# Kernel tuning notes

Measured on AMD Instinct MI355X. Metric: run time of the kernel, lower is better.

## Reference

```python
import jax, jax.numpy as jnp
import numpy as np

N_USER, N_ITEM, N_REL = 200000, 100000, 64
DIM = 64
S_UU = S_UI = S_IU = S_II = 8
BATCH = 65536
MAX_RATING = 5.0


def setup_inputs() -> dict:
    key = jax.random.key(0)
    ks = jax.random.split(key, 24)
    inp = {}
    # query batch
    inp['u'] = jax.random.randint(ks[0], (BATCH,), 0, N_USER)
    inp['v'] = jax.random.randint(ks[1], (BATCH,), 0, N_ITEM)
    # embedding tables (init std=0.8 as in the torch code)
    inp['usr_feat'] = 0.8 * jax.random.normal(ks[2], (N_USER, DIM), jnp.float32)
    inp['item_feat'] = 0.8 * jax.random.normal(ks[3], (N_ITEM, DIM), jnp.float32)
    inp['rel_feat'] = 0.8 * jax.random.normal(ks[4], (N_REL, DIM), jnp.float32)
    # precomputed sampled neighbor tables (built once in __init__ in the original)
    inp['neigh_uu'] = jax.random.randint(ks[5], (N_USER, S_UU), 0, N_USER)
    inp['neigh_uu_st'] = jax.random.uniform(ks[6], (N_USER, S_UU), jnp.float32)
    inp['neigh_ui'] = jax.random.randint(ks[7], (N_USER, S_UI), 0, N_ITEM)
    inp['neigh_ui_rat'] = MAX_RATING * jax.random.uniform(ks[8], (N_USER, S_UI), jnp.float32)
    inp['neigh_ui_vot'] = jax.random.uniform(ks[9], (N_USER, S_UI), jnp.float32)
    inp['neigh_ui_tim'] = jax.random.uniform(ks[10], (N_USER, S_UI), jnp.float32)
    inp['neigh_iu'] = jax.random.randint(ks[11], (N_ITEM, S_IU), 0, N_USER)
    inp['neigh_iu_rat'] = MAX_RATING * jax.random.uniform(ks[12], (N_ITEM, S_IU), jnp.float32)
    inp['neigh_iu_vot'] = jax.random.uniform(ks[13], (N_ITEM, S_IU), jnp.float32)
    inp['neigh_iu_tim'] = jax.random.uniform(ks[14], (N_ITEM, S_IU), jnp.float32)
    inp['neigh_ii'] = jax.random.randint(ks[15], (N_ITEM, S_II), 0, N_ITEM)
    inp['neigh_ir'] = jax.random.randint(ks[16], (N_ITEM, S_II), 0, N_REL)
    # aggregator transforms (one per side)
    sc = 1.0 / np.sqrt(DIM)
    inp['Wu'] = sc * jax.random.normal(ks[17], (DIM, DIM), jnp.float32)
    inp['bu'] = jnp.zeros((DIM,), jnp.float32)
    inp['Wv'] = sc * jax.random.normal(ks[18], (DIM, DIM), jnp.float32)
    inp['bv'] = jnp.zeros((DIM,), jnp.float32)
    return inp


def reference(u, v, usr_feat, item_feat, rel_feat,
              neigh_uu, neigh_uu_st, neigh_ui, neigh_ui_rat, neigh_ui_vot, neigh_ui_tim,
              neigh_iu, neigh_iu_rat, neigh_iu_vot, neigh_iu_tim, neigh_ii, neigh_ir,
              Wu, bu, Wv, bv):
    u_emb = usr_feat[u]                                   # [B, D]
    v_emb = item_feat[v]                                  # [B, D]

    # ---- user-side aggregation ----
    # social neighbors, weighted by softmax over social tie strength
    uu_nei = usr_feat[neigh_uu[u]]                        # [B, S, D]
    w_uu = jax.nn.softmax(neigh_uu_st[u], axis=-1)        # [B, S]
    agg_uu = jnp.einsum('bs,bsd->bd', w_uu, uu_nei)
    # interacted items, weighted by rating * vote * time recency
    ui_nei = item_feat[neigh_ui[u]]                       # [B, S, D]
    s_ui = neigh_ui_rat[u] * neigh_ui_vot[u] * neigh_ui_tim[u]
    w_ui = jax.nn.softmax(s_ui, axis=-1)
    agg_ui = jnp.einsum('bs,bsd->bd', w_ui, ui_nei)
    user_h = jax.nn.relu((u_emb + agg_uu + agg_ui) @ Wu + bu)

    # ---- item-side aggregation ----
    # users who interacted with the item, weighted like above
    iu_nei = usr_feat[neigh_iu[v]]                        # [B, S, D]
    s_iu = neigh_iu_rat[v] * neigh_iu_vot[v] * neigh_iu_tim[v]
    w_iu = jax.nn.softmax(s_iu, axis=-1)
    agg_iu = jnp.einsum('bs,bsd->bd', w_iu, iu_nei)
    # KG neighbors with user-relation attention (KGCN-style)
    ii_nei = item_feat[neigh_ii[v]]                       # [B, S, D]
    rel = rel_feat[neigh_ir[v]]                           # [B, S, D]
    att = jnp.einsum('bd,bsd->bs', u_emb, rel)            # user-relation score
    w_ii = jax.nn.softmax(att, axis=-1)
    agg_ii = jnp.einsum('bs,bsd->bd', w_ii, ii_nei)
    item_h = jax.nn.relu((v_emb + agg_iu + agg_ii) @ Wv + bv)

    # rating prediction
    score = jax.nn.sigmoid(jnp.sum(user_h * item_h, axis=-1)) * MAX_RATING
    return score
```

## Files before the change

kernel.cpp:

```cpp
#include <hip/hip_runtime.h>
#include <math.h>

constexpr int DIM = 64;
constexpr int S = 8;
constexpr int WPB = 4;
constexpr int BLOCK = WPB * 64;
constexpr int GRID = 2048;

constexpr int N_USER = 200000;
constexpr int N_ITEM = 100000;
constexpr size_t USR16_BYTES  = (size_t)N_USER * DIM * 2;
constexpr size_t ITEM16_BYTES = (size_t)N_ITEM * DIM * 2;
constexpr size_t WS_NEEDED    = USR16_BYTES + ITEM16_BYTES;

typedef __attribute__((ext_vector_type(8))) __bf16 bf16x8;
typedef __attribute__((ext_vector_type(4))) float  f32x4;
typedef __attribute__((ext_vector_type(8))) float     f32x8;
typedef __attribute__((ext_vector_type(8))) _Float16  f16x8;

#define LDS_FENCE() asm volatile("s_waitcnt lgkmcnt(0)" ::: "memory")
#define SCHED_PIN() __builtin_amdgcn_sched_barrier(0)

template <int CTRL>
__device__ __forceinline__ float dppx(float x) {
    return __builtin_bit_cast(float,
        __builtin_amdgcn_mov_dpp(__builtin_bit_cast(int, x), CTRL, 0xf, 0xf, true));
}
#define XOR1 0xB1
#define XOR2 0x4E

__device__ __forceinline__ unsigned pk_bf16(float a, float b) {
    unsigned ua = __builtin_bit_cast(unsigned, a);
    unsigned ub = __builtin_bit_cast(unsigned, b);
    ua = (ua + 0x8000u) >> 16;
    ub = (ub + 0x8000u) & 0xffff0000u;
    return ua | ub;
}

__device__ __forceinline__ void octet_softmax(float sc, float* wout) {
    float m = sc;
    m = fmaxf(m, dppx<XOR1>(m));
    m = fmaxf(m, dppx<XOR2>(m));
    m = fmaxf(m, __shfl_xor(m, 4));
    float e = __expf(sc - m);
    float s = e;
    s += dppx<XOR1>(s);
    s += dppx<XOR2>(s);
    s += __shfl_xor(s, 4);
    float w = e / s;
    #pragma unroll
    for (int k = 0; k < 8; k++) wout[k] = __shfl(w, k);
}

__device__ __forceinline__ void matvec_h(
    float xv, int lane, unsigned short* xw,
    const bf16x8* xa00, const bf16x8* xa01,
    const bf16x8* xa10, const bf16x8* xa11,
    const unsigned* bf,
    float b0, float b1, float b2, float b3,
    float& h0, float& h1, float& h2, float& h3)
{
    LDS_FENCE();
    const unsigned xb = __builtin_bit_cast(unsigned, xv);
    const unsigned hb = (xb + 0x8000u) & 0xffff0000u;
    const float xl = xv - __builtin_bit_cast(float, hb);
    xw[lane]      = (unsigned short)(hb >> 16);
    xw[64 + lane] = (unsigned short)((__builtin_bit_cast(unsigned, xl) + 0x8000u) >> 16);
    LDS_FENCE();

    f32x4 a0 = {0.f, 0.f, 0.f, 0.f};
    f32x4 a1 = a0, a2 = a0, a3 = a0;

    {
        const bf16x8 ah = *xa00, al = *xa01;
        const bf16x8 w0 = *(const bf16x8*)(bf);
        const bf16x8 w1 = *(const bf16x8*)(bf + 256);
        const bf16x8 w2 = *(const bf16x8*)(bf + 512);
        const bf16x8 w3 = *(const bf16x8*)(bf + 768);
        a0 = __builtin_amdgcn_mfma_f32_16x16x32_bf16(ah, w0, a0, 0, 0, 0);
        a0 = __builtin_amdgcn_mfma_f32_16x16x32_bf16(al, w0, a0, 0, 0, 0);
        a1 = __builtin_amdgcn_mfma_f32_16x16x32_bf16(ah, w1, a1, 0, 0, 0);
        a1 = __builtin_amdgcn_mfma_f32_16x16x32_bf16(al, w1, a1, 0, 0, 0);
        a2 = __builtin_amdgcn_mfma_f32_16x16x32_bf16(ah, w2, a2, 0, 0, 0);
        a2 = __builtin_amdgcn_mfma_f32_16x16x32_bf16(al, w2, a2, 0, 0, 0);
        a3 = __builtin_amdgcn_mfma_f32_16x16x32_bf16(ah, w3, a3, 0, 0, 0);
        a3 = __builtin_amdgcn_mfma_f32_16x16x32_bf16(al, w3, a3, 0, 0, 0);
    }
    {
        const bf16x8 ah = *xa10, al = *xa11;
        const bf16x8 w0 = *(const bf16x8*)(bf + 1024);
        const bf16x8 w1 = *(const bf16x8*)(bf + 1280);
        const bf16x8 w2 = *(const bf16x8*)(bf + 1536);
        const bf16x8 w3 = *(const bf16x8*)(bf + 1792);
        a0 = __builtin_amdgcn_mfma_f32_16x16x32_bf16(ah, w0, a0, 0, 0, 0);
        a0 = __builtin_amdgcn_mfma_f32_16x16x32_bf16(al, w0, a0, 0, 0, 0);
        a1 = __builtin_amdgcn_mfma_f32_16x16x32_bf16(ah, w1, a1, 0, 0, 0);
        a1 = __builtin_amdgcn_mfma_f32_16x16x32_bf16(al, w1, a1, 0, 0, 0);
        a2 = __builtin_amdgcn_mfma_f32_16x16x32_bf16(ah, w2, a2, 0, 0, 0);
        a2 = __builtin_amdgcn_mfma_f32_16x16x32_bf16(al, w2, a2, 0, 0, 0);
        a3 = __builtin_amdgcn_mfma_f32_16x16x32_bf16(ah, w3, a3, 0, 0, 0);
        a3 = __builtin_amdgcn_mfma_f32_16x16x32_bf16(al, w3, a3, 0, 0, 0);
    }

    h0 = fmaxf(a0[0] + b0, 0.f);
    h1 = fmaxf(a1[0] + b1, 0.f);
    h2 = fmaxf(a2[0] + b2, 0.f);
    h3 = fmaxf(a3[0] + b3, 0.f);
}

__global__ __launch_bounds__(256)
void cvt16_kernel(const float* __restrict__ usr_feat, const float* __restrict__ item_feat,
                  _Float16* __restrict__ usr16, _Float16* __restrict__ item16,
                  int n8u, int n8t)
{
    const int i = blockIdx.x * 256 + threadIdx.x;
    if (i >= n8t) return;
    const float* src = (i < n8u) ? usr_feat : item_feat;
    _Float16*   dst = (i < n8u) ? usr16    : item16;
    const int j = (i < n8u) ? i : (i - n8u);
    const f32x8 v = ((const f32x8*)src)[j];
    ((f16x8*)dst)[j] = __builtin_convertvector(v, f16x8);
}

template <bool USE16>
__global__ __launch_bounds__(BLOCK, 4)
void sestkgcn_kernel(
    const int*   __restrict__ u_idx,
    const int*   __restrict__ v_idx,
    const float* __restrict__ usr_feat,
    const float* __restrict__ item_feat,
    const float* __restrict__ rel_feat,
    const int*   __restrict__ neigh_uu,
    const float* __restrict__ neigh_uu_st,
    const int*   __restrict__ neigh_ui,
    const float* __restrict__ neigh_ui_rat,
    const float* __restrict__ neigh_ui_vot,
    const float* __restrict__ neigh_ui_tim,
    const int*   __restrict__ neigh_iu,
    const float* __restrict__ neigh_iu_rat,
    const float* __restrict__ neigh_iu_vot,
    const float* __restrict__ neigh_iu_tim,
    const int*   __restrict__ neigh_ii,
    const int*   __restrict__ neigh_ir,
    const float* __restrict__ Wu,
    const float* __restrict__ bu,
    const float* __restrict__ Wv,
    const float* __restrict__ bv,
    const _Float16* __restrict__ usr16,
    const _Float16* __restrict__ item16,
    float*       __restrict__ out,
    int n)
{
    __shared__ unsigned sBFu[2048];
    __shared__ unsigned sBFv[2048];
    __shared__ __align__(16) unsigned short sX[WPB][128];

    const int tid = threadIdx.x;
    for (int i = tid; i < 2048; i += BLOCK) {
        const int d = i & 3, l = (i >> 2) & 63, f = i >> 8;
        const int row = ((f >> 2) << 5) + ((l >> 4) << 3) + (d << 1);
        const int col = ((f & 3) << 4) + (l & 15);
        sBFu[i] = pk_bf16(Wu[row * DIM + col], Wu[(row + 1) * DIM + col]);
        sBFv[i] = pk_bf16(Wv[row * DIM + col], Wv[(row + 1) * DIM + col]);
    }
    __syncthreads();

    const int wave = tid >> 6;
    const int lane = tid & 63;
    const int ls   = lane & 7;
    const int g    = lane >> 4;
    const int c    = lane & 15;

    unsigned short* xw = &sX[wave][0];
    const bf16x8* xa00 = (const bf16x8*)&sX[wave][g * 8];
    const bf16x8* xa01 = (const bf16x8*)&sX[wave][64 + g * 8];
    const bf16x8* xa10 = (const bf16x8*)&sX[wave][32 + g * 8];
    const bf16x8* xa11 = (const bf16x8*)&sX[wave][96 + g * 8];
    const unsigned* bfu = &sBFu[lane * 4];
    const unsigned* bfv = &sBFv[lane * 4];

    const float bu0 = bu[c], bu1 = bu[c + 16], bu2 = bu[c + 32], bu3 = bu[c + 48];
    const float bv0 = bv[c], bv1 = bv[c + 16], bv2 = bv[c + 32], bv3 = bv[c + 48];

    const int stride = GRID * WPB;
    int b = blockIdx.x * WPB + wave;
    if (b >= n) return;

    int u = u_idx[b], v = v_idx[b];
    int bc1 = b + stride; if (bc1 >= n) bc1 = b;
    int u1 = u_idx[bc1], v1 = v_idx[bc1];

    unsigned u8 = (unsigned)u << 3, v8 = (unsigned)v << 3;
    int4 iuu0 = ((const int4*)(neigh_uu + u8))[0];
    int4 iuu1 = ((const int4*)(neigh_uu + u8))[1];
    int4 iui0 = ((const int4*)(neigh_ui + u8))[0];
    int4 iui1 = ((const int4*)(neigh_ui + u8))[1];
    int4 iiu0 = ((const int4*)(neigh_iu + v8))[0];
    int4 iiu1 = ((const int4*)(neigh_iu + v8))[1];
    int4 iii0 = ((const int4*)(neigh_ii + v8))[0];
    int4 iii1 = ((const int4*)(neigh_ii + v8))[1];
    int4 iir0 = ((const int4*)(neigh_ir + v8))[0];
    int4 iir1 = ((const int4*)(neigh_ir + v8))[1];
    float suu_r = neigh_uu_st[u8 + ls];
    float uir = neigh_ui_rat[u8 + ls], uiv = neigh_ui_vot[u8 + ls], uit = neigh_ui_tim[u8 + ls];
    float iur = neigh_iu_rat[v8 + ls], ivv = neigh_iu_vot[v8 + ls], ivt = neigh_iu_tim[v8 + ls];
    float ud_c = usr_feat[((unsigned)u << 6) | (unsigned)lane];
    float vd_c = item_feat[((unsigned)v << 6) | (unsigned)lane];
    float ruu[S], rui[S], riu[S], rii[S];
    {
        const int nuu[S] = {iuu0.x, iuu0.y, iuu0.z, iuu0.w, iuu1.x, iuu1.y, iuu1.z, iuu1.w};
        const int nui[S] = {iui0.x, iui0.y, iui0.z, iui0.w, iui1.x, iui1.y, iui1.z, iui1.w};
        const int niu[S] = {iiu0.x, iiu0.y, iiu0.z, iiu0.w, iiu1.x, iiu1.y, iiu1.z, iiu1.w};
        const int nii[S] = {iii0.x, iii0.y, iii0.z, iii0.w, iii1.x, iii1.y, iii1.z, iii1.w};
        #pragma unroll
        for (int s = 0; s < S; s++) {
            const unsigned ix = ((unsigned)nuu[s] << 6) | (unsigned)lane;
            ruu[s] = USE16 ? (float)usr16[ix] : usr_feat[ix];
        }
        #pragma unroll
        for (int s = 0; s < S; s++) {
            const unsigned ix = ((unsigned)nui[s] << 6) | (unsigned)lane;
            rui[s] = USE16 ? (float)item16[ix] : item_feat[ix];
        }
        #pragma unroll
        for (int s = 0; s < S; s++) {
            const unsigned ix = ((unsigned)niu[s] << 6) | (unsigned)lane;
            riu[s] = USE16 ? (float)usr16[ix] : usr_feat[ix];
        }
        #pragma unroll
        for (int s = 0; s < S; s++) {
            const unsigned ix = ((unsigned)nii[s] << 6) | (unsigned)lane;
            rii[s] = USE16 ? (float)item16[ix] : item_feat[ix];
        }
    }
    float ud_n = 0.f, vd_n = 0.f;

    while (true) {
        float rr[S];
        {
            const int nir[S] = {iir0.x, iir0.y, iir0.z, iir0.w, iir1.x, iir1.y, iir1.z, iir1.w};
            #pragma unroll
            for (int s = 0; s < S; s++) rr[s] = rel_feat[((unsigned)nir[s] << 6) | (unsigned)lane];
        }
        const unsigned u81 = (unsigned)u1 << 3, v81 = (unsigned)v1 << 3;
        iuu0 = ((const int4*)(neigh_uu + u81))[0];
        iuu1 = ((const int4*)(neigh_uu + u81))[1];
        iui0 = ((const int4*)(neigh_ui + u81))[0];
        iui1 = ((const int4*)(neigh_ui + u81))[1];
        iiu0 = ((const int4*)(neigh_iu + v81))[0];
        iiu1 = ((const int4*)(neigh_iu + v81))[1];
        iii0 = ((const int4*)(neigh_ii + v81))[0];
        iii1 = ((const int4*)(neigh_ii + v81))[1];
        iir0 = ((const int4*)(neigh_ir + v81))[0];
        iir1 = ((const int4*)(neigh_ir + v81))[1];
        int b2c = b + 2 * stride; if (b2c >= n) b2c = b;
        const int u2 = u_idx[b2c], v2 = v_idx[b2c];
        SCHED_PIN();

        float w[S];
        octet_softmax(suu_r, w);
        float agg_uu = 0.f;
        #pragma unroll
        for (int s = 0; s < S; s++) agg_uu = fmaf(w[s], ruu[s], agg_uu);

        octet_softmax(uir * uiv * uit, w);
        float agg_ui = 0.f;
        #pragma unroll
        for (int s = 0; s < S; s++) agg_ui = fmaf(w[s], rui[s], agg_ui);

        float hu0, hu1, hu2, hu3;
        matvec_h(ud_c + agg_uu + agg_ui, lane, xw, xa00, xa01, xa10, xa11,
                 bfu, bu0, bu1, bu2, bu3, hu0, hu1, hu2, hu3);

        octet_softmax(iur * ivv * ivt, w);
        float agg_iu = 0.f;
        #pragma unroll
        for (int s = 0; s < S; s++) agg_iu = fmaf(w[s], riu[s], agg_iu);

        {
            float p[S];
            #pragma unroll
            for (int s = 0; s < S; s++) p[s] = ud_c * rr[s];

            float m1[4];
            #pragma unroll
            for (int i = 0; i < 4; i++) {
                float lo = (lane & 1) ? p[2 * i + 1] : p[2 * i];
                float hi = (lane & 1) ? p[2 * i]     : p[2 * i + 1];
                m1[i] = lo + dppx<XOR1>(hi);
            }
            float m2[2];
            #pragma unroll
            for (int i = 0; i < 2; i++) {
                float lo = (lane & 2) ? m1[2 * i + 1] : m1[2 * i];
                float hi = (lane & 2) ? m1[2 * i]     : m1[2 * i + 1];
                m2[i] = lo + dppx<XOR2>(hi);
            }
            float lo = (lane & 4) ? m2[1] : m2[0];
            float hi = (lane & 4) ? m2[0] : m2[1];
            float att = lo + __shfl_xor(hi, 4);
            att += __shfl_xor(att, 8);
            att += __shfl_xor(att, 16);
            att += __shfl_xor(att, 32);
            octet_softmax(att, w);
        }
        float agg_ii = 0.f;
        #pragma unroll
        for (int s = 0; s < S; s++) agg_ii = fmaf(w[s], rii[s], agg_ii);

        {
            const int nuu[S] = {iuu0.x, iuu0.y, iuu0.z, iuu0.w, iuu1.x, iuu1.y, iuu1.z, iuu1.w};
            const int nui[S] = {iui0.x, iui0.y, iui0.z, iui0.w, iui1.x, iui1.y, iui1.z, iui1.w};
            const int niu[S] = {iiu0.x, iiu0.y, iiu0.z, iiu0.w, iiu1.x, iiu1.y, iiu1.z, iiu1.w};
            const int nii[S] = {iii0.x, iii0.y, iii0.z, iii0.w, iii1.x, iii1.y, iii1.z, iii1.w};
            #pragma unroll
            for (int s = 0; s < S; s++) {
                const unsigned ix = ((unsigned)nuu[s] << 6) | (unsigned)lane;
                ruu[s] = USE16 ? (float)usr16[ix] : usr_feat[ix];
            }
            #pragma unroll
            for (int s = 0; s < S; s++) {
                const unsigned ix = ((unsigned)nui[s] << 6) | (unsigned)lane;
                rui[s] = USE16 ? (float)item16[ix] : item_feat[ix];
            }
            #pragma unroll
            for (int s = 0; s < S; s++) {
                const unsigned ix = ((unsigned)niu[s] << 6) | (unsigned)lane;
                riu[s] = USE16 ? (float)usr16[ix] : usr_feat[ix];
            }
            #pragma unroll
            for (int s = 0; s < S; s++) {
                const unsigned ix = ((unsigned)nii[s] << 6) | (unsigned)lane;
                rii[s] = USE16 ? (float)item16[ix] : item_feat[ix];
            }
        }
        suu_r = neigh_uu_st[u81 + ls];
        uir = neigh_ui_rat[u81 + ls]; uiv = neigh_ui_vot[u81 + ls]; uit = neigh_ui_tim[u81 + ls];
        iur = neigh_iu_rat[v81 + ls]; ivv = neigh_iu_vot[v81 + ls]; ivt = neigh_iu_tim[v81 + ls];
        ud_n = usr_feat[((unsigned)u1 << 6) | (unsigned)lane];
        vd_n = item_feat[((unsigned)v1 << 6) | (unsigned)lane];
        SCHED_PIN();

        float hv0, hv1, hv2, hv3;
        matvec_h(vd_c + agg_iu + agg_ii, lane, xw, xa00, xa01, xa10, xa11,
                 bfv, bv0, bv1, bv2, bv3, hv0, hv1, hv2, hv3);

        float p = hu0 * hv0 + hu1 * hv1 + hu2 * hv2 + hu3 * hv3;
        p += dppx<XOR1>(p);
        p += dppx<XOR2>(p);
        p += __shfl_xor(p, 4);
        p += __shfl_xor(p, 8);
        if (lane == 0) out[b] = 5.0f / (1.0f + __expf(-p));

        b += stride;
        if (b >= n) break;
        u = u1; v = v1; u1 = u2; v1 = v2;
        ud_c = ud_n; vd_c = vd_n;
    }
}

extern "C" void kernel_launch(void* const* d_in, const int* in_sizes, int n_in,
                              void* d_out, int out_size, void* d_ws, size_t ws_size,
                              hipStream_t stream) {
    const int*   u_idx        = (const int*)  d_in[0];
    const int*   v_idx        = (const int*)  d_in[1];
    const float* usr_feat     = (const float*)d_in[2];
    const float* item_feat    = (const float*)d_in[3];
    const float* rel_feat     = (const float*)d_in[4];
    const int*   neigh_uu     = (const int*)  d_in[5];
    const float* neigh_uu_st  = (const float*)d_in[6];
    const int*   neigh_ui     = (const int*)  d_in[7];
    const float* neigh_ui_rat = (const float*)d_in[8];
    const float* neigh_ui_vot = (const float*)d_in[9];
    const float* neigh_ui_tim = (const float*)d_in[10];
    const int*   neigh_iu     = (const int*)  d_in[11];
    const float* neigh_iu_rat = (const float*)d_in[12];
    const float* neigh_iu_vot = (const float*)d_in[13];
    const float* neigh_iu_tim = (const float*)d_in[14];
    const int*   neigh_ii     = (const int*)  d_in[15];
    const int*   neigh_ir     = (const int*)  d_in[16];
    const float* Wu           = (const float*)d_in[17];
    const float* bu           = (const float*)d_in[18];
    const float* Wv           = (const float*)d_in[19];
    const float* bv           = (const float*)d_in[20];
    float*       out          = (float*)d_out;

    const int n = in_sizes[0];
    int blocks = (n + WPB - 1) / WPB;
    if (blocks > GRID) blocks = GRID;

    const bool use16 = (d_ws != nullptr) && (ws_size >= WS_NEEDED);
    if (use16) {
        _Float16* usr16  = (_Float16*)d_ws;
        _Float16* item16 = (_Float16*)((char*)d_ws + USR16_BYTES);
        const int n8u = N_USER * DIM / 8;
        const int n8t = n8u + N_ITEM * DIM / 8;
        cvt16_kernel<<<(n8t + 255) / 256, 256, 0, stream>>>(
            usr_feat, item_feat, usr16, item16, n8u, n8t);
        sestkgcn_kernel<true><<<blocks, BLOCK, 0, stream>>>(
            u_idx, v_idx, usr_feat, item_feat, rel_feat,
            neigh_uu, neigh_uu_st, neigh_ui, neigh_ui_rat, neigh_ui_vot, neigh_ui_tim,
            neigh_iu, neigh_iu_rat, neigh_iu_vot, neigh_iu_tim, neigh_ii, neigh_ir,
            Wu, bu, Wv, bv, usr16, item16, out, n);
    } else {
        sestkgcn_kernel<false><<<blocks, BLOCK, 0, stream>>>(
            u_idx, v_idx, usr_feat, item_feat, rel_feat,
            neigh_uu, neigh_uu_st, neigh_ui, neigh_ui_rat, neigh_ui_vot, neigh_ui_tim,
            neigh_iu, neigh_iu_rat, neigh_iu_vot, neigh_iu_tim, neigh_ii, neigh_ir,
            Wu, bu, Wv, bv, nullptr, nullptr, out, n);
    }
}
```

Baseline: 265.5 us.

## Gather neighbor rows as lane-pairs with half-wave neighbor split

Reorganizes the neighbor gathers so each lane loads two adjacent dims (a dword of fp16 or a float2), and the two half-waves each handle four of the eight neighbors. Partial sums are combined with a cross-half shuffle, and the LDS staging of the matvec input is rewritten to write packed pairs. This halves the number of gather load instructions and the register footprint of prefetched rows. The cost is extra shuffles for the weights, the half-wave reduction and redistributing the user embedding.

```diff
diff --git a/kernel.cpp b/kernel.cpp
--- a/kernel.cpp
+++ b/kernel.cpp
@@ -17,6 +17,7 @@
 typedef __attribute__((ext_vector_type(4))) float  f32x4;
 typedef __attribute__((ext_vector_type(8))) float     f32x8;
 typedef __attribute__((ext_vector_type(8))) _Float16  f16x8;
+typedef __attribute__((ext_vector_type(2))) _Float16  f16x2;
 
 #define LDS_FENCE() asm volatile("s_waitcnt lgkmcnt(0)" ::: "memory")
 #define SCHED_PIN() __builtin_amdgcn_sched_barrier(0)
@@ -37,7 +38,7 @@
     return ua | ub;
 }
 
-__device__ __forceinline__ void octet_softmax(float sc, float* wout) {
+__device__ __forceinline__ void octet_softmax_pair(float sc, int half, float* wt) {
     float m = sc;
     m = fmaxf(m, dppx<XOR1>(m));
     m = fmaxf(m, dppx<XOR2>(m));
@@ -49,25 +50,71 @@
     s += __shfl_xor(s, 4);
     float w = e / s;
     #pragma unroll
-    for (int k = 0; k < 8; k++) wout[k] = __shfl(w, k);
-}
-
-__device__ __forceinline__ void matvec_h(
-    float xv, int lane, unsigned short* xw,
+    for (int t = 0; t < 4; t++) wt[t] = __shfl(w, 2 * t + half);
+}
+
+template <bool USE16>
+__device__ __forceinline__ void pair_gather(
+    const float* tbl32, const _Float16* tbl16,
+    int4 i0, int4 i1, int half, int dw, uint2* pd)
+{
+    const int n0 = half ? i0.y : i0.x;
+    const int n1 = half ? i0.w : i0.z;
+    const int n2 = half ? i1.y : i1.x;
+    const int n3 = half ? i1.w : i1.z;
+    if constexpr (USE16) {
+        pd[0].x = ((const unsigned*)(tbl16 + ((unsigned)n0 << 6)))[dw];
+        pd[1].x = ((const unsigned*)(tbl16 + ((unsigned)n1 << 6)))[dw];
+        pd[2].x = ((const unsigned*)(tbl16 + ((unsigned)n2 << 6)))[dw];
+        pd[3].x = ((const unsigned*)(tbl16 + ((unsigned)n3 << 6)))[dw];
+    } else {
+        pd[0] = ((const uint2*)(tbl32 + ((unsigned)n0 << 6)))[dw];
+        pd[1] = ((const uint2*)(tbl32 + ((unsigned)n1 << 6)))[dw];
+        pd[2] = ((const uint2*)(tbl32 + ((unsigned)n2 << 6)))[dw];
+        pd[3] = ((const uint2*)(tbl32 + ((unsigned)n3 << 6)))[dw];
+    }
+}
+
+template <bool USE16>
+__device__ __forceinline__ float2 unpk(uint2 p) {
+    if constexpr (USE16) {
+        const f16x2 h = __builtin_bit_cast(f16x2, p.x);
+        return make_float2((float)h[0], (float)h[1]);
+    } else {
+        return make_float2(__builtin_bit_cast(float, p.x), __builtin_bit_cast(float, p.y));
+    }
+}
+
+template <bool USE16>
+__device__ __forceinline__ void pair_fma(const uint2* pd, const float* wt, float& aL, float& aH) {
+    #pragma unroll
+    for (int t = 0; t < 4; t++) {
+        const float2 r = unpk<USE16>(pd[t]);
+        aL = fmaf(wt[t], r.x, aL);
+        aH = fmaf(wt[t], r.y, aH);
+    }
+}
+
+__device__ __forceinline__ void stage_x_pair(float xL, float xH, int dw, unsigned short* xw) {
+    LDS_FENCE();
+    const unsigned bL  = __builtin_bit_cast(unsigned, xL);
+    const unsigned hbL = (bL + 0x8000u) & 0xffff0000u;
+    const unsigned bH  = __builtin_bit_cast(unsigned, xH);
+    const unsigned hbH = (bH + 0x8000u) & 0xffff0000u;
+    const float rL = xL - __builtin_bit_cast(float, hbL);
+    const float rH = xH - __builtin_bit_cast(float, hbH);
+    ((unsigned*)xw)[dw]      = (hbL >> 16) | hbH;
+    ((unsigned*)xw)[32 + dw] = pk_bf16(rL, rH);
+    LDS_FENCE();
+}
+
+__device__ __forceinline__ void matvec_core(
     const bf16x8* xa00, const bf16x8* xa01,
     const bf16x8* xa10, const bf16x8* xa11,
     const unsigned* bf,
     float b0, float b1, float b2, float b3,
     float& h0, float& h1, float& h2, float& h3)
 {
-    LDS_FENCE();
-    const unsigned xb = __builtin_bit_cast(unsigned, xv);
-    const unsigned hb = (xb + 0x8000u) & 0xffff0000u;
-    const float xl = xv - __builtin_bit_cast(float, hb);
-    xw[lane]      = (unsigned short)(hb >> 16);
-    xw[64 + lane] = (unsigned short)((__builtin_bit_cast(unsigned, xl) + 0x8000u) >> 16);
-    LDS_FENCE();
-
     f32x4 a0 = {0.f, 0.f, 0.f, 0.f};
     f32x4 a1 = a0, a2 = a0, a3 = a0;
 
@@ -170,6 +217,8 @@
     const int ls   = lane & 7;
     const int g    = lane >> 4;
     const int c    = lane & 15;
+    const int half = lane >> 5;
+    const int dw   = lane & 31;
 
     unsigned short* xw = &sX[wave][0];
     const bf16x8* xa00 = (const bf16x8*)&sX[wave][g * 8];
@@ -205,35 +254,14 @@
     float uir = neigh_ui_rat[u8 + ls], uiv = neigh_ui_vot[u8 + ls], uit = neigh_ui_tim[u8 + ls];
     float iur = neigh_iu_rat[v8 + ls], ivv = neigh_iu_vot[v8 + ls], ivt = neigh_iu_tim[v8 + ls];
     float ud_c = usr_feat[((unsigned)u << 6) | (unsigned)lane];
-    float vd_c = item_feat[((unsigned)v << 6) | (unsigned)lane];
-    float ruu[S], rui[S], riu[S], rii[S];
-    {
-        const int nuu[S] = {iuu0.x, iuu0.y, iuu0.z, iuu0.w, iuu1.x, iuu1.y, iuu1.z, iuu1.w};
-        const int nui[S] = {iui0.x, iui0.y, iui0.z, iui0.w, iui1.x, iui1.y, iui1.z, iui1.w};
-        const int niu[S] = {iiu0.x, iiu0.y, iiu0.z, iiu0.w, iiu1.x, iiu1.y, iiu1.z, iiu1.w};
-        const int nii[S] = {iii0.x, iii0.y, iii0.z, iii0.w, iii1.x, iii1.y, iii1.z, iii1.w};
-        #pragma unroll
-        for (int s = 0; s < S; s++) {
-            const unsigned ix = ((unsigned)nuu[s] << 6) | (unsigned)lane;
-            ruu[s] = USE16 ? (float)usr16[ix] : usr_feat[ix];
-        }
-        #pragma unroll
-        for (int s = 0; s < S; s++) {
-            const unsigned ix = ((unsigned)nui[s] << 6) | (unsigned)lane;
-            rui[s] = USE16 ? (float)item16[ix] : item_feat[ix];
-        }
-        #pragma unroll
-        for (int s = 0; s < S; s++) {
-            const unsigned ix = ((unsigned)niu[s] << 6) | (unsigned)lane;
-            riu[s] = USE16 ? (float)usr16[ix] : usr_feat[ix];
-        }
-        #pragma unroll
-        for (int s = 0; s < S; s++) {
-            const unsigned ix = ((unsigned)nii[s] << 6) | (unsigned)lane;
-            rii[s] = USE16 ? (float)item16[ix] : item_feat[ix];
-        }
-    }
-    float ud_n = 0.f, vd_n = 0.f;
+    float2 vd_c = ((const float2*)(item_feat + ((unsigned)v << 6)))[dw];
+    uint2 pdu_uu[4], pdu_ui[4], pdi_iu[4], pdi_ii[4];
+    pair_gather<USE16>(usr_feat,  usr16,  iuu0, iuu1, half, dw, pdu_uu);
+    pair_gather<USE16>(item_feat, item16, iui0, iui1, half, dw, pdu_ui);
+    pair_gather<USE16>(usr_feat,  usr16,  iiu0, iiu1, half, dw, pdi_iu);
+    pair_gather<USE16>(item_feat, item16, iii0, iii1, half, dw, pdi_ii);
+    float  ud_n = 0.f;
+    float2 vd_n = make_float2(0.f, 0.f);
 
     while (true) {
         float rr[S];
@@ -257,25 +285,27 @@
         const int u2 = u_idx[b2c], v2 = v_idx[b2c];
         SCHED_PIN();
 
-        float w[S];
-        octet_softmax(suu_r, w);
-        float agg_uu = 0.f;
-        #pragma unroll
-        for (int s = 0; s < S; s++) agg_uu = fmaf(w[s], ruu[s], agg_uu);
-
-        octet_softmax(uir * uiv * uit, w);
-        float agg_ui = 0.f;
-        #pragma unroll
-        for (int s = 0; s < S; s++) agg_ui = fmaf(w[s], rui[s], agg_ui);
+        float wt[4];
+        float sumL, sumH;
+        {
+            octet_softmax_pair(suu_r, half, wt);
+            float aL = 0.f, aH = 0.f;
+            pair_fma<USE16>(pdu_uu, wt, aL, aH);
+            octet_softmax_pair(uir * uiv * uit, half, wt);
+            pair_fma<USE16>(pdu_ui, wt, aL, aH);
+            sumL = aL + __shfl_xor(aL, 32);
+            sumH = aH + __shfl_xor(aH, 32);
+        }
+        const float udL = __shfl(ud_c, 2 * dw);
+        const float udH = __shfl(ud_c, 2 * dw + 1);
 
         float hu0, hu1, hu2, hu3;
-        matvec_h(ud_c + agg_uu + agg_ui, lane, xw, xa00, xa01, xa10, xa11,
-                 bfu, bu0, bu1, bu2, bu3, hu0, hu1, hu2, hu3);
-
-        octet_softmax(iur * ivv * ivt, w);
-        float agg_iu = 0.f;
-        #pragma unroll
-        for (int s = 0; s < S; s++) agg_iu = fmaf(w[s], riu[s], agg_iu);
+        stage_x_pair(udL + sumL, udH + sumH, dw, xw);
+        matvec_core(xa00, xa01, xa10, xa11, bfu, bu0, bu1, bu2, bu3, hu0, hu1, hu2, hu3);
+
+        float aL = 0.f, aH = 0.f;
+        octet_softmax_pair(iur * ivv * ivt, half, wt);
+        pair_fma<USE16>(pdi_iu, wt, aL, aH);
 
         {
             float p[S];
@@ -302,48 +332,26 @@
             att += __shfl_xor(att, 8);
             att += __shfl_xor(att, 16);
             att += __shfl_xor(att, 32);
-            octet_softmax(att, w);
+            octet_softmax_pair(att, half, wt);
         }
-        float agg_ii = 0.f;
-        #pragma unroll
-        for (int s = 0; s < S; s++) agg_ii = fmaf(w[s], rii[s], agg_ii);
-
-        {
-            const int nuu[S] = {iuu0.x, iuu0.y, iuu0.z, iuu0.w, iuu1.x, iuu1.y, iuu1.z, iuu1.w};
-            const int nui[S] = {iui0.x, iui0.y, iui0.z, iui0.w, iui1.x, iui1.y, iui1.z, iui1.w};
-            const int niu[S] = {iiu0.x, iiu0.y, iiu0.z, iiu0.w, iiu1.x, iiu1.y, iiu1.z, iiu1.w};
-            const int nii[S] = {iii0.x, iii0.y, iii0.z, iii0.w, iii1.x, iii1.y, iii1.z, iii1.w};
-            #pragma unroll
-            for (int s = 0; s < S; s++) {
-                const unsigned ix = ((unsigned)nuu[s] << 6) | (unsigned)lane;
-                ruu[s] = USE16 ? (float)usr16[ix] : usr_feat[ix];
-            }
-            #pragma unroll
-            for (int s = 0; s < S; s++) {
-                const unsigned ix = ((unsigned)nui[s] << 6) | (unsigned)lane;
-                rui[s] = USE16 ? (float)item16[ix] : item_feat[ix];
-            }
-            #pragma unroll
-            for (int s = 0; s < S; s++) {
-                const unsigned ix = ((unsigned)niu[s] << 6) | (unsigned)lane;
-                riu[s] = USE16 ? (float)usr16[ix] : usr_feat[ix];
-            }
-            #pragma unroll
-            for (int s = 0; s < S; s++) {
-                const unsigned ix = ((unsigned)nii[s] << 6) | (unsigned)lane;
-                rii[s] = USE16 ? (float)item16[ix] : item_feat[ix];
-            }
-        }
+        pair_fma<USE16>(pdi_ii, wt, aL, aH);
+        sumL = aL + __shfl_xor(aL, 32);
+        sumH = aH + __shfl_xor(aH, 32);
+
+        pair_gather<USE16>(usr_feat,  usr16,  iuu0, iuu1, half, dw, pdu_uu);
+        pair_gather<USE16>(item_feat, item16, iui0, iui1, half, dw, pdu_ui);
+        pair_gather<USE16>(usr_feat,  usr16,  iiu0, iiu1, half, dw, pdi_iu);
+        pair_gather<USE16>(item_feat, item16, iii0, iii1, half, dw, pdi_ii);
         suu_r = neigh_uu_st[u81 + ls];
         uir = neigh_ui_rat[u81 + ls]; uiv = neigh_ui_vot[u81 + ls]; uit = neigh_ui_tim[u81 + ls];
         iur = neigh_iu_rat[v81 + ls]; ivv = neigh_iu_vot[v81 + ls]; ivt = neigh_iu_tim[v81 + ls];
         ud_n = usr_feat[((unsigned)u1 << 6) | (unsigned)lane];
-        vd_n = item_feat[((unsigned)v1 << 6) | (unsigned)lane];
+        vd_n = ((const float2*)(item_feat + ((unsigned)v1 << 6)))[dw];
         SCHED_PIN();
 
         float hv0, hv1, hv2, hv3;
-        matvec_h(vd_c + agg_iu + agg_ii, lane, xw, xa00, xa01, xa10, xa11,
-                 bfv, bv0, bv1, bv2, bv3, hv0, hv1, hv2, hv3);
+        stage_x_pair(vd_c.x + sumL, vd_c.y + sumH, dw, xw);
+        matvec_core(xa00, xa01, xa10, xa11, bfv, bv0, bv1, bv2, bv3, hv0, hv1, hv2, hv3);
 
         float p = hu0 * hv0 + hu1 * hv1 + hu2 * hv2 + hu3 * hv3;
         p += dppx<XOR1>(p);
```

Result: slower. 277.3 us (+4.4%).
